# Performance work log

Hardware: AMD Instinct MI355X
Metric: run time of the kernel (lower is better)

The kernel has to match this reference:

```python
import jax, jax.numpy as jnp
import numpy as np

B = 512
MIRROR_C1_OFFSET = -1.2432432432432432

def make_ff(batch):
    ff = jnp.zeros((1, 1, 60, 60), jnp.float32)
    ff = ff.at[0, 0, :, 41:51].set(0.5)
    ff = ff.at[0, 0, :, 51:].set(1.0)
    return jnp.broadcast_to(ff, (batch, 1, 60, 60))

def conv_valid(x, w, b):
    y = jax.lax.conv_general_dilated(x, w, (1, 1), 'VALID',
                                     dimension_numbers=('NCHW', 'OIHW', 'NCHW'))
    return y + b[None, :, None, None]

def build_padded(x, h, ff):
    # (B,3,92,92) canvas with custom mirror padding (channel-dependent sign on left)
    b = x.shape[0]
    inner = jnp.concatenate([x, h, ff], axis=1)  # (B,3,60,60)
    h2 = jnp.zeros((b, 3, 92, 92), x.dtype)
    h2 = h2.at[:, :, 16:76, 16:76].set(inner)
    h2 = h2.at[:, :, 16:76, 76:].set(h2[:, :, 16:76, 60:76][..., ::-1])
    h2 = h2.at[:, :, 76:, 16:].set(h2[:, :, 60:76, 16:][:, :, ::-1, :])
    h2 = h2.at[:, :, :16, 16:].set(0.0)
    left = h2[:, :, :, 16:32][..., ::-1]  # mirror across col 16
    h2 = h2.at[:, 0, :, :16].set(left[:, 0])
    h2 = h2.at[:, 2, :, :16].set(left[:, 2])
    h2 = h2.at[:, 1, :, :16].set(MIRROR_C1_OFFSET - left[:, 1])
    return h2

def powerlayer(x, h, ff, w1, b1, w2, b2, w3, b3, w4, b4):
    h2 = build_padded(x, h, ff)
    h2 = jax.nn.relu(conv_valid(h2, w1, b1))  # (B,8,84,84)
    h2 = jax.nn.relu(conv_valid(h2, w2, b2))  # (B,8,76,76)
    h2 = jax.nn.relu(conv_valid(h2, w3, b3))  # (B,8,68,68)
    h2 = conv_valid(h2, w4, b4)               # (B,1,60,60)
    return h2

def setup_inputs() -> dict:
    key = jax.random.key(0)
    ks = jax.random.split(key, 10)
    x = jax.random.normal(ks[0], (B, 1, 60, 60), jnp.float32)
    fc_w = jax.random.normal(ks[1], (3600, 3600), jnp.float32) * (1.0 / 60.0)
    fc_b = jax.random.normal(ks[2], (3600,), jnp.float32) * 0.01
    w1 = jax.random.normal(ks[3], (8, 3, 9, 9), jnp.float32) * (1.0 / np.sqrt(3 * 81))
    bC1 = jnp.zeros((8,), jnp.float32)
    w2 = jax.random.normal(ks[4], (8, 8, 9, 9), jnp.float32) * (1.0 / np.sqrt(8 * 81))
    bC2 = jnp.zeros((8,), jnp.float32)
    w3 = jax.random.normal(ks[5], (8, 8, 9, 9), jnp.float32) * (1.0 / np.sqrt(8 * 81))
    bC3 = jnp.zeros((8,), jnp.float32)
    w4 = jax.random.normal(ks[6], (1, 8, 9, 9), jnp.float32) * (1.0 / np.sqrt(8 * 81))
    bC4 = jnp.zeros((1,), jnp.float32)
    return {"x": x, "fc_w": fc_w, "fc_b": fc_b,
            "w1": w1, "bC1": bC1, "w2": w2, "bC2": bC2,
            "w3": w3, "bC3": bC3, "w4": w4, "bC4": bC4}

def reference(x, fc_w, fc_b, w1, bC1, w2, bC2, w3, bC3, w4, bC4):
    b = x.shape[0]
    ff = make_ff(b)
    h = jax.nn.relu(x.reshape(b, 3600) @ fc_w.T + fc_b)
    h = h.reshape(b, 1, 60, 60)
    for _ in range(5):
        h = powerlayer(x, h, ff, w1, bC1, w2, bC2, w3, bC3, w4, bC4)
    return h.reshape(b, 60, 60)
```

## Files before the change

kernel.cpp:

```cpp
#include <hip/hip_runtime.h>

#define B_IMG 512
#define C1OFF (-1.2432432432432432f)

typedef __attribute__((ext_vector_type(2))) float f2;
typedef __attribute__((ext_vector_type(2), aligned(4))) float f2u;
typedef __attribute__((ext_vector_type(4))) float f4;
typedef __attribute__((ext_vector_type(4), aligned(4))) float f4u;

__device__ __forceinline__ float relu_(float v) { return v > 0.f ? v : 0.f; }
__device__ __forceinline__ f2 mk2(float a, float b) { f2 r; r[0] = a; r[1] = b; return r; }

__device__ __forceinline__ int swz_block(int bid, int nwg) {
    int q = nwg >> 3, r = nwg & 7;
    int xcd = bid & 7, idx = bid >> 3;
    return (xcd < r ? xcd * (q + 1) : r * (q + 1) + (xcd - r) * q) + idx;
}

__device__ __forceinline__ f2 pk_fma_sb0(f2 acc, f2 a, f2 b) {
    asm("v_pk_fma_f32 %0, %1, %2, %0 op_sel:[0,0,0] op_sel_hi:[0,1,1]"
        : "+v"(acc) : "s"(a), "v"(b));
    return acc;
}
__device__ __forceinline__ f2 pk_fma_sb1(f2 acc, f2 a, f2 b) {
    asm("v_pk_fma_f32 %0, %1, %2, %0 op_sel:[1,0,0] op_sel_hi:[1,1,1]"
        : "+v"(acc) : "s"(a), "v"(b));
    return acc;
}
__device__ __forceinline__ f2 pk_fma_vb0(f2 acc, f2 a, f2 b) {
    asm("v_pk_fma_f32 %0, %1, %2, %0 op_sel:[0,0,0] op_sel_hi:[0,1,1]"
        : "+v"(acc) : "v"(a), "v"(b));
    return acc;
}
__device__ __forceinline__ f2 pk_fma_vb1(f2 acc, f2 a, f2 b) {
    asm("v_pk_fma_f32 %0, %1, %2, %0 op_sel:[1,0,0] op_sel_hi:[1,1,1]"
        : "+v"(acc) : "v"(a), "v"(b));
    return acc;
}

__global__ __launch_bounds__(256) void fc_kernel(
    const float* __restrict__ X, const float* __restrict__ W,
    const float* __restrict__ Bv, float* __restrict__ H)
{
    __shared__ __align__(16) float As[16][68];
    __shared__ __align__(16) float Bs[16][68];
    const int tid = threadIdx.x;
    const int m0 = blockIdx.y * 64;
    const int n0 = blockIdx.x * 64;
    const int tm = tid >> 4, tn = tid & 15;
    const int lr = tid >> 2;
    const int lk = (tid & 3) << 2;
    const bool bvalid = (n0 + lr) < 3600;
    const float* Arow = X + (size_t)(m0 + lr) * 3600 + lk;
    const float* Brow = W + (size_t)(bvalid ? (n0 + lr) : 0) * 3600 + lk;
    f2 acc2[4][2] = {};
    for (int k0 = 0; k0 < 3600; k0 += 16) {
        float4 av = *(const float4*)(Arow + k0);
        float4 bv = make_float4(0.f, 0.f, 0.f, 0.f);
        if (bvalid) bv = *(const float4*)(Brow + k0);
        __syncthreads();
        As[lk + 0][lr] = av.x; As[lk + 1][lr] = av.y;
        As[lk + 2][lr] = av.z; As[lk + 3][lr] = av.w;
        Bs[lk + 0][lr] = bv.x; Bs[lk + 1][lr] = bv.y;
        Bs[lk + 2][lr] = bv.z; Bs[lk + 3][lr] = bv.w;
        __syncthreads();
        #pragma unroll
        for (int kk = 0; kk < 16; ++kk) {
            f2 a01 = *(const f2*)&As[kk][tm << 2];
            f2 a23 = *(const f2*)&As[kk][(tm << 2) + 2];
            f2 b01 = *(const f2*)&Bs[kk][tn << 2];
            f2 b23 = *(const f2*)&Bs[kk][(tn << 2) + 2];
            acc2[0][0] = pk_fma_vb0(acc2[0][0], a01, b01);
            acc2[0][1] = pk_fma_vb0(acc2[0][1], a01, b23);
            acc2[1][0] = pk_fma_vb1(acc2[1][0], a01, b01);
            acc2[1][1] = pk_fma_vb1(acc2[1][1], a01, b23);
            acc2[2][0] = pk_fma_vb0(acc2[2][0], a23, b01);
            acc2[2][1] = pk_fma_vb0(acc2[2][1], a23, b23);
            acc2[3][0] = pk_fma_vb1(acc2[3][0], a23, b01);
            acc2[3][1] = pk_fma_vb1(acc2[3][1], a23, b23);
        }
    }
    #pragma unroll
    for (int i = 0; i < 4; ++i) {
        int m = m0 + (tm << 2) + i;
        float vals[4] = { acc2[i][0][0], acc2[i][0][1],
                          acc2[i][1][0], acc2[i][1][1] };
        #pragma unroll
        for (int j = 0; j < 4; ++j) {
            int n = n0 + (tn << 2) + j;
            if (n < 3600)
                H[(size_t)m * 3600 + n] = relu_(vals[j] + Bv[n]);
        }
    }
}

__global__ __launch_bounds__(256) void prep_pk(
    const float* __restrict__ w, int OC, int IC, f2* __restrict__ out)
{
    int n = IC * 9 * OC * 5;
    for (int t = threadIdx.x + blockIdx.x * 256; t < n; t += gridDim.x * 256) {
        int m = t % 5; int rest = t / 5;
        int oc = rest % OC; rest /= OC;
        int ky = rest % 9; int ic = rest / 9;
        const float* ws = w + (((size_t)oc * IC + ic) * 9 + ky) * 9;
        float lo = ws[2 * m];
        float hi = (2 * m + 1 < 9) ? ws[2 * m + 1] : 0.f;
        out[t] = mk2(lo, hi);
    }
}

__device__ __forceinline__ float pad_core(const float* __restrict__ xb,
                                          const float* __restrict__ hb,
                                          int ch, int r, int c)
{
    if (r < 16) return 0.f;
    int rr = (r <= 75) ? r : (151 - r);
    int cc = (c <= 75) ? c : (151 - c);
    int i = rr - 16, j = cc - 16;
    if (ch == 0) return xb[i * 60 + j];
    if (ch == 1) return hb[i * 60 + j];
    return (j >= 51) ? 1.0f : ((j >= 41) ? 0.5f : 0.0f);
}

__device__ __forceinline__ float pad_val(const float* __restrict__ xb,
                                         const float* __restrict__ hb,
                                         int ch, int r, int c)
{
    if (c >= 16) return pad_core(xb, hb, ch, r, c);
    float v = pad_core(xb, hb, ch, r, 31 - c);
    return (ch == 1) ? (C1OFF - v) : v;
}

__global__ __launch_bounds__(256) void pad_kernel(
    const float* __restrict__ x, const float* __restrict__ h,
    float* __restrict__ pad)
{
    const int b = blockIdx.x;
    const float* xb = x + (size_t)b * 3600;
    const float* hb = h + (size_t)b * 3600;
    float* pb = pad + (size_t)b * (3 * 92 * 92);
    for (int i = threadIdx.x; i < 3 * 92 * 92; i += 256) {
        int ch = i / 8464;
        int rem = i - ch * 8464;
        int r = rem / 92;
        int c = rem - r * 92;
        pb[i] = pad_val(xb, hb, ch, r, c);
    }
}

template<int IC, int OC, int IH, bool RELU>
__global__ __launch_bounds__(256, 3) void convP(
    const float* __restrict__ in, const f2* __restrict__ wpk,
    const float* __restrict__ bias, float* __restrict__ out, int total)
{
    constexpr int IW = IH, OH = IH - 8, OW = OH;
    constexpr int NGX = OW / 4, NPB = OH * NGX;
    const int sb = swz_block(blockIdx.x, gridDim.x);
    const int p0 = sb * 256 + threadIdx.x;
    const bool act = (p0 < total);
    const int p = act ? p0 : (total - 1);
    const int b = p / NPB;
    const int rem = p - b * NPB;
    const int oy = rem / NGX;
    const int x0 = (rem - oy * NGX) * 4;
    const float* ib = in + (size_t)b * IC * IH * IW + (size_t)oy * IW + x0;

    f2 acc[OC][2];
    #pragma unroll
    for (int oc = 0; oc < OC; ++oc) {
        float bv = bias[oc];
        acc[oc][0] = mk2(bv, bv);
        acc[oc][1] = mk2(bv, bv);
    }

    #pragma unroll 1
    for (int ic = 0; ic < IC; ++ic) {
        const float* rp = ib + (size_t)ic * IH * IW;
        const f2* wq0 = wpk + (size_t)ic * 9 * OC * 5;
        #pragma unroll
        for (int ky = 0; ky < 9; ++ky) {
            const float* row = rp + ky * IW;
            f4 e0 = *(const f4*)(row);
            f4 e1 = *(const f4*)(row + 4);
            f4 e2 = *(const f4*)(row + 8);
            f4u s0 = *(const f4u*)(row + 1);
            f4u s1 = *(const f4u*)(row + 5);
            f2u s2 = *(const f2u*)(row + 9);
            f2 re[6], sh[5];
            re[0] = mk2(e0[0], e0[1]); re[1] = mk2(e0[2], e0[3]);
            re[2] = mk2(e1[0], e1[1]); re[3] = mk2(e1[2], e1[3]);
            re[4] = mk2(e2[0], e2[1]); re[5] = mk2(e2[2], e2[3]);
            sh[0] = mk2(s0[0], s0[1]); sh[1] = mk2(s0[2], s0[3]);
            sh[2] = mk2(s1[0], s1[1]); sh[3] = mk2(s1[2], s1[3]);
            sh[4] = mk2(s2[0], s2[1]);
            const f2* wq = wq0 + ky * OC * 5;
            #pragma unroll
            for (int oc = 0; oc < OC; ++oc) {
                const f2* w5 = wq + oc * 5;
                #pragma unroll
                for (int m = 0; m < 4; ++m) {
                    f2 w = w5[m];
                    acc[oc][0] = pk_fma_sb0(acc[oc][0], w, re[m]);
                    acc[oc][0] = pk_fma_sb1(acc[oc][0], w, sh[m]);
                    acc[oc][1] = pk_fma_sb0(acc[oc][1], w, re[m + 1]);
                    acc[oc][1] = pk_fma_sb1(acc[oc][1], w, sh[m + 1]);
                }
                f2 w4v = w5[4];
                acc[oc][0] = pk_fma_sb0(acc[oc][0], w4v, re[4]);
                acc[oc][1] = pk_fma_sb0(acc[oc][1], w4v, re[5]);
            }
        }
    }

    if (act) {
        #pragma unroll
        for (int oc = 0; oc < OC; ++oc) {
            float* ob = out + ((size_t)b * OC + oc) * (OH * OW)
                        + (size_t)oy * OW + x0;
            float v0 = acc[oc][0][0], v1 = acc[oc][0][1];
            float v2 = acc[oc][1][0], v3 = acc[oc][1][1];
            if (RELU) { v0 = relu_(v0); v1 = relu_(v1); v2 = relu_(v2); v3 = relu_(v3); }
            *(float4*)ob = make_float4(v0, v1, v2, v3);
        }
    }
}

extern "C" void kernel_launch(void* const* d_in, const int* in_sizes, int n_in,
                              void* d_out, int out_size, void* d_ws, size_t ws_size,
                              hipStream_t stream)
{
    const float* x   = (const float*)d_in[0];
    const float* fcw = (const float*)d_in[1];
    const float* fcb = (const float*)d_in[2];
    const float* w1  = (const float*)d_in[3];
    const float* b1  = (const float*)d_in[4];
    const float* w2  = (const float*)d_in[5];
    const float* b2  = (const float*)d_in[6];
    const float* w3  = (const float*)d_in[7];
    const float* b3  = (const float*)d_in[8];
    const float* w4  = (const float*)d_in[9];
    const float* b4  = (const float*)d_in[10];

    float* h = (float*)d_out;

    f2* wp1 = (f2*)d_ws;
    f2* wp2 = wp1 + 4096;
    f2* wp3 = wp2 + 4096;
    f2* wp4 = wp3 + 4096;
    float* fbase = (float*)((char*)d_ws + 131072);
    size_t avail = (ws_size - 131072) / sizeof(float);

    const size_t PADN = 3 * 92 * 92;
    const size_t T1N  = 8 * 84 * 84;
    const size_t T2N  = 8 * 76 * 76;
    size_t per_img = PADN + T1N + T2N;
    int CH = (int)(avail / per_img);
    if (CH > B_IMG) CH = B_IMG;
    if (CH < 1) CH = 1;
    float* pad = fbase;
    float* t1  = pad + (size_t)CH * PADN;
    float* t2  = t1 + (size_t)CH * T1N;

    prep_pk<<<5, 256, 0, stream>>>(w1, 8, 3, wp1);
    prep_pk<<<12, 256, 0, stream>>>(w2, 8, 8, wp2);
    prep_pk<<<12, 256, 0, stream>>>(w3, 8, 8, wp3);
    prep_pk<<<2, 256, 0, stream>>>(w4, 1, 8, wp4);

    fc_kernel<<<dim3(57, 8), 256, 0, stream>>>(x, fcw, fcb, h);

    for (int it = 0; it < 5; ++it) {
        for (int c0 = 0; c0 < B_IMG; c0 += CH) {
            int cn = (B_IMG - c0) < CH ? (B_IMG - c0) : CH;
            pad_kernel<<<cn, 256, 0, stream>>>(x + (size_t)c0 * 3600,
                                               h + (size_t)c0 * 3600, pad);
            int t1n = cn * 1764, t2n = cn * 1444, t3n = cn * 1156, t4n = cn * 900;
            convP<3, 8, 92, true><<<(t1n + 255) / 256, 256, 0, stream>>>(
                pad, wp1, b1, t1, t1n);
            convP<8, 8, 84, true><<<(t2n + 255) / 256, 256, 0, stream>>>(
                t1, wp2, b2, t2, t2n);
            convP<8, 8, 76, true><<<(t3n + 255) / 256, 256, 0, stream>>>(
                t2, wp3, b3, t1, t3n);
            convP<8, 1, 68, false><<<(t4n + 255) / 256, 256, 0, stream>>>(
                t1, wp4, b4, h + (size_t)c0 * 3600, t4n);
        }
    }
}
```

Baseline: 3.972 ms.

## Compute two output rows per thread with rolling input-row register reuse

```diff
diff --git a/kernel.cpp b/kernel.cpp
--- a/kernel.cpp
+++ b/kernel.cpp
@@ -148,68 +148,93 @@
     }
 }
 
+#define LOADROW(RE, SH, KY)                                                   \
+    do {                                                                      \
+        const float* row_ = rp + (KY) * IW;                                   \
+        f4 e0_ = *(const f4*)(row_);                                          \
+        f4 e1_ = *(const f4*)(row_ + 4);                                      \
+        f4 e2_ = *(const f4*)(row_ + 8);                                      \
+        f4u s0_ = *(const f4u*)(row_ + 1);                                    \
+        f4u s1_ = *(const f4u*)(row_ + 5);                                    \
+        f2u s2_ = *(const f2u*)(row_ + 9);                                    \
+        RE[0] = mk2(e0_[0], e0_[1]); RE[1] = mk2(e0_[2], e0_[3]);             \
+        RE[2] = mk2(e1_[0], e1_[1]); RE[3] = mk2(e1_[2], e1_[3]);             \
+        RE[4] = mk2(e2_[0], e2_[1]); RE[5] = mk2(e2_[2], e2_[3]);             \
+        SH[0] = mk2(s0_[0], s0_[1]); SH[1] = mk2(s0_[2], s0_[3]);             \
+        SH[2] = mk2(s1_[0], s1_[1]); SH[3] = mk2(s1_[2], s1_[3]);             \
+        SH[4] = mk2(s2_[0], s2_[1]);                                          \
+    } while (0)
+
+#define FMASTEP(TRE, TSH, BRE, BSH, KY)                                       \
+    do {                                                                      \
+        const f2* wq_ = wq0 + (KY) * OC * 5;                                  \
+        _Pragma("unroll")                                                     \
+        for (int oc = 0; oc < OC; ++oc) {                                     \
+            const f2* w5_ = wq_ + oc * 5;                                     \
+            _Pragma("unroll")                                                 \
+            for (int m = 0; m < 4; ++m) {                                     \
+                f2 w_ = w5_[m];                                               \
+                acc[oc][0][0] = pk_fma_sb0(acc[oc][0][0], w_, TRE[m]);        \
+                acc[oc][0][0] = pk_fma_sb1(acc[oc][0][0], w_, TSH[m]);        \
+                acc[oc][0][1] = pk_fma_sb0(acc[oc][0][1], w_, TRE[m + 1]);    \
+                acc[oc][0][1] = pk_fma_sb1(acc[oc][0][1], w_, TSH[m + 1]);    \
+                acc[oc][1][0] = pk_fma_sb0(acc[oc][1][0], w_, BRE[m]);        \
+                acc[oc][1][0] = pk_fma_sb1(acc[oc][1][0], w_, BSH[m]);        \
+                acc[oc][1][1] = pk_fma_sb0(acc[oc][1][1], w_, BRE[m + 1]);    \
+                acc[oc][1][1] = pk_fma_sb1(acc[oc][1][1], w_, BSH[m + 1]);    \
+            }                                                                 \
+            f2 w4_ = w5_[4];                                                  \
+            acc[oc][0][0] = pk_fma_sb0(acc[oc][0][0], w4_, TRE[4]);           \
+            acc[oc][0][1] = pk_fma_sb0(acc[oc][0][1], w4_, TRE[5]);           \
+            acc[oc][1][0] = pk_fma_sb0(acc[oc][1][0], w4_, BRE[4]);           \
+            acc[oc][1][1] = pk_fma_sb0(acc[oc][1][1], w4_, BRE[5]);           \
+        }                                                                     \
+    } while (0)
+
+#define STEP(TRE, TSH, BRE, BSH, KY)                                          \
+    do { LOADROW(BRE, BSH, (KY) + 1); FMASTEP(TRE, TSH, BRE, BSH, KY); } while (0)
+
 template<int IC, int OC, int IH, bool RELU>
-__global__ __launch_bounds__(256, 3) void convP(
+__global__ __launch_bounds__(256, 2) void convP2(
     const float* __restrict__ in, const f2* __restrict__ wpk,
     const float* __restrict__ bias, float* __restrict__ out, int total)
 {
     constexpr int IW = IH, OH = IH - 8, OW = OH;
-    constexpr int NGX = OW / 4, NPB = OH * NGX;
+    constexpr int NGX = OW / 4, NGY = OH / 2, NPB = NGX * NGY;
     const int sb = swz_block(blockIdx.x, gridDim.x);
     const int p0 = sb * 256 + threadIdx.x;
     const bool act = (p0 < total);
     const int p = act ? p0 : (total - 1);
     const int b = p / NPB;
     const int rem = p - b * NPB;
-    const int oy = rem / NGX;
-    const int x0 = (rem - oy * NGX) * 4;
+    const int gy = rem / NGX;
+    const int gx = rem - gy * NGX;
+    const int oy = gy * 2, x0 = gx * 4;
     const float* ib = in + (size_t)b * IC * IH * IW + (size_t)oy * IW + x0;
 
-    f2 acc[OC][2];
+    f2 acc[OC][2][2];
     #pragma unroll
     for (int oc = 0; oc < OC; ++oc) {
         float bv = bias[oc];
-        acc[oc][0] = mk2(bv, bv);
-        acc[oc][1] = mk2(bv, bv);
+        acc[oc][0][0] = mk2(bv, bv); acc[oc][0][1] = mk2(bv, bv);
+        acc[oc][1][0] = mk2(bv, bv); acc[oc][1][1] = mk2(bv, bv);
     }
 
     #pragma unroll 1
     for (int ic = 0; ic < IC; ++ic) {
         const float* rp = ib + (size_t)ic * IH * IW;
         const f2* wq0 = wpk + (size_t)ic * 9 * OC * 5;
-        #pragma unroll
-        for (int ky = 0; ky < 9; ++ky) {
-            const float* row = rp + ky * IW;
-            f4 e0 = *(const f4*)(row);
-            f4 e1 = *(const f4*)(row + 4);
-            f4 e2 = *(const f4*)(row + 8);
-            f4u s0 = *(const f4u*)(row + 1);
-            f4u s1 = *(const f4u*)(row + 5);
-            f2u s2 = *(const f2u*)(row + 9);
-            f2 re[6], sh[5];
-            re[0] = mk2(e0[0], e0[1]); re[1] = mk2(e0[2], e0[3]);
-            re[2] = mk2(e1[0], e1[1]); re[3] = mk2(e1[2], e1[3]);
-            re[4] = mk2(e2[0], e2[1]); re[5] = mk2(e2[2], e2[3]);
-            sh[0] = mk2(s0[0], s0[1]); sh[1] = mk2(s0[2], s0[3]);
-            sh[2] = mk2(s1[0], s1[1]); sh[3] = mk2(s1[2], s1[3]);
-            sh[4] = mk2(s2[0], s2[1]);
-            const f2* wq = wq0 + ky * OC * 5;
-            #pragma unroll
-            for (int oc = 0; oc < OC; ++oc) {
-                const f2* w5 = wq + oc * 5;
-                #pragma unroll
-                for (int m = 0; m < 4; ++m) {
-                    f2 w = w5[m];
-                    acc[oc][0] = pk_fma_sb0(acc[oc][0], w, re[m]);
-                    acc[oc][0] = pk_fma_sb1(acc[oc][0], w, sh[m]);
-                    acc[oc][1] = pk_fma_sb0(acc[oc][1], w, re[m + 1]);
-                    acc[oc][1] = pk_fma_sb1(acc[oc][1], w, sh[m + 1]);
-                }
-                f2 w4v = w5[4];
-                acc[oc][0] = pk_fma_sb0(acc[oc][0], w4v, re[4]);
-                acc[oc][1] = pk_fma_sb0(acc[oc][1], w4v, re[5]);
-            }
-        }
+        f2 reA[6], shA[5], reB[6], shB[5];
+        LOADROW(reA, shA, 0);
+        STEP(reA, shA, reB, shB, 0);
+        STEP(reB, shB, reA, shA, 1);
+        STEP(reA, shA, reB, shB, 2);
+        STEP(reB, shB, reA, shA, 3);
+        STEP(reA, shA, reB, shB, 4);
+        STEP(reB, shB, reA, shA, 5);
+        STEP(reA, shA, reB, shB, 6);
+        STEP(reB, shB, reA, shA, 7);
+        STEP(reA, shA, reB, shB, 8);
     }
 
     if (act) {
@@ -217,10 +242,16 @@
         for (int oc = 0; oc < OC; ++oc) {
             float* ob = out + ((size_t)b * OC + oc) * (OH * OW)
                         + (size_t)oy * OW + x0;
-            float v0 = acc[oc][0][0], v1 = acc[oc][0][1];
-            float v2 = acc[oc][1][0], v3 = acc[oc][1][1];
-            if (RELU) { v0 = relu_(v0); v1 = relu_(v1); v2 = relu_(v2); v3 = relu_(v3); }
-            *(float4*)ob = make_float4(v0, v1, v2, v3);
+            float v0 = acc[oc][0][0][0], v1 = acc[oc][0][0][1];
+            float v2 = acc[oc][0][1][0], v3 = acc[oc][0][1][1];
+            float u0 = acc[oc][1][0][0], u1 = acc[oc][1][0][1];
+            float u2 = acc[oc][1][1][0], u3 = acc[oc][1][1][1];
+            if (RELU) {
+                v0 = relu_(v0); v1 = relu_(v1); v2 = relu_(v2); v3 = relu_(v3);
+                u0 = relu_(u0); u1 = relu_(u1); u2 = relu_(u2); u3 = relu_(u3);
+            }
+            *(float4*)&ob[0]  = make_float4(v0, v1, v2, v3);
+            *(float4*)&ob[OW] = make_float4(u0, u1, u2, u3);
         }
     }
 }
@@ -273,14 +304,14 @@
             int cn = (B_IMG - c0) < CH ? (B_IMG - c0) : CH;
             pad_kernel<<<cn, 256, 0, stream>>>(x + (size_t)c0 * 3600,
                                                h + (size_t)c0 * 3600, pad);
-            int t1n = cn * 1764, t2n = cn * 1444, t3n = cn * 1156, t4n = cn * 900;
-            convP<3, 8, 92, true><<<(t1n + 255) / 256, 256, 0, stream>>>(
+            int t1n = cn * 882, t2n = cn * 722, t3n = cn * 578, t4n = cn * 450;
+            convP2<3, 8, 92, true><<<(t1n + 255) / 256, 256, 0, stream>>>(
                 pad, wp1, b1, t1, t1n);
-            convP<8, 8, 84, true><<<(t2n + 255) / 256, 256, 0, stream>>>(
+            convP2<8, 8, 84, true><<<(t2n + 255) / 256, 256, 0, stream>>>(
                 t1, wp2, b2, t2, t2n);
-            convP<8, 8, 76, true><<<(t3n + 255) / 256, 256, 0, stream>>>(
+            convP2<8, 8, 76, true><<<(t3n + 255) / 256, 256, 0, stream>>>(
                 t2, wp3, b3, t1, t3n);
-            convP<8, 1, 68, false><<<(t4n + 255) / 256, 256, 0, stream>>>(
+            convP2<8, 1, 68, false><<<(t4n + 255) / 256, 256, 0, stream>>>(
                 t1, wp4, b4, h + (size_t)c0 * 3600, t4n);
         }
     }
```

Result: no change. 3.900 ms (-1.8%).
